# Performance work log

Measured on AMD Instinct MI355X. Metric: run time of the kernel, lower is better.

Reference implementation:

```python
import jax, jax.numpy as jnp
import numpy as np

T, C, H = 2048, 1024, 16
D = C // H  # head dim = 64


def setup_inputs() -> dict:
    key = jax.random.key(0)
    k1, k2, k3 = jax.random.split(key, 3)
    x = jax.random.normal(k1, (T, C), dtype=jnp.float32)
    W_qkv = jax.random.normal(k2, (C, 3 * C), dtype=jnp.float32) * (1.0 / np.sqrt(C))
    b_qkv = jnp.zeros((3 * C,), dtype=jnp.float32)
    W_proj = jax.random.normal(k3, (C, C), dtype=jnp.float32) * (1.0 / np.sqrt(C))
    b_proj = jnp.zeros((C,), dtype=jnp.float32)
    return {"x": x, "W_qkv": W_qkv, "b_qkv": b_qkv, "W_proj": W_proj, "b_proj": b_proj}


def reference(x, W_qkv, b_qkv, W_proj, b_proj):
    t, c = x.shape
    qkv = x @ W_qkv + b_qkv                      # [T, 3C] fused QKV projection
    q, k, v = jnp.split(qkv, 3, axis=-1)         # each [T, C]
    # split heads: [T, C] -> [H, T, D]
    q = q.reshape(t, H, D).transpose(1, 0, 2)
    k = k.reshape(t, H, D).transpose(1, 0, 2)
    v = v.reshape(t, H, D).transpose(1, 0, 2)
    # naive O(T^2) attention, full score matrix [H, T, T]
    att = jnp.einsum('htd,hsd->hts', q, k) / jnp.sqrt(jnp.float32(D))
    att = jax.nn.softmax(att, axis=-1)
    y = jnp.einsum('hts,hsd->htd', att, v)       # [H, T, D]
    y = y.transpose(1, 0, 2).reshape(t, c)       # merge heads -> [T, C]
    return y @ W_proj + b_proj
```

## Files before the change

### kernel.cpp

```cpp
#include <hip/hip_runtime.h>
#include <hip/hip_bf16.h>
#include <stdint.h>

#define T_DIM 2048
#define C_DIM 1024
#define H_DIM 16
#define D_HEAD 64
#define N_QKV 3072
#define CQ 0.18033688011112042f

typedef __bf16 bf16;
typedef __bf16 bf16x8 __attribute__((ext_vector_type(8)));
typedef __bf16 bf16x4 __attribute__((ext_vector_type(4)));
typedef __bf16 bf16x2 __attribute__((ext_vector_type(2)));
typedef float f32x4 __attribute__((ext_vector_type(4)));
typedef short s16x4 __attribute__((ext_vector_type(4)));

__device__ __forceinline__ void lds_load16(const void* g, void* l) {
    __builtin_amdgcn_global_load_lds(
        (const __attribute__((address_space(1))) void*)g,
        (__attribute__((address_space(3))) void*)l, 16, 0, 0);
}

__device__ __forceinline__ f32x4 mfma16(bf16x4 a, bf16x4 b, f32x4 c) {
#if __has_builtin(__builtin_amdgcn_mfma_f32_16x16x16_bf16)
    return __builtin_amdgcn_mfma_f32_16x16x16_bf16(a, b, c, 0, 0, 0);
#elif __has_builtin(__builtin_amdgcn_mfma_f32_16x16x16bf16_1k)
    union { bf16x4 v; s16x4 s; } ua, ub;
    ua.v = a; ub.v = b;
    return __builtin_amdgcn_mfma_f32_16x16x16bf16_1k(ua.s, ub.s, c, 0, 0, 0);
#else
    asm volatile("v_mfma_f32_16x16x16_bf16 %0, %1, %2, %0"
                 : "+v"(c) : "v"(a), "v"(b));
    return c;
#endif
}

__global__ void prep_kernel(const float* __restrict__ x, bf16* __restrict__ xb,
                            const float* __restrict__ Wq, bf16* __restrict__ WqT,
                            const float* __restrict__ Wp, bf16* __restrict__ WpT) {
    __shared__ float tile[32][33];
    int bid = blockIdx.x;
    int t = threadIdx.x;
    if (bid < 1024) {
        int i = (bid * 256 + t) * 8;
        float4 a = *(const float4*)(x + i);
        float4 b = *(const float4*)(x + i + 4);
        bf16x8 o;
        o[0] = (bf16)a.x; o[1] = (bf16)a.y; o[2] = (bf16)a.z; o[3] = (bf16)a.w;
        o[4] = (bf16)b.x; o[5] = (bf16)b.y; o[6] = (bf16)b.z; o[7] = (bf16)b.w;
        *(bf16x8*)(xb + i) = o;
        return;
    }
    bid -= 1024;
    const float* in; bf16* out; int N, nb, kb;
    if (bid < 3072) { in = Wq; out = WqT; N = N_QKV; nb = (bid % 96) * 32; kb = (bid / 96) * 32; }
    else { bid -= 3072; in = Wp; out = WpT; N = C_DIM; nb = (bid % 32) * 32; kb = (bid / 32) * 32; }
    int r = t >> 3, c4 = (t & 7) * 4;
    float4 v = *(const float4*)(in + (size_t)(kb + r) * N + nb + c4);
    tile[r][c4 + 0] = v.x; tile[r][c4 + 1] = v.y;
    tile[r][c4 + 2] = v.z; tile[r][c4 + 3] = v.w;
    __syncthreads();
    bf16x4 ov;
    ov[0] = (bf16)tile[c4 + 0][r]; ov[1] = (bf16)tile[c4 + 1][r];
    ov[2] = (bf16)tile[c4 + 2][r]; ov[3] = (bf16)tile[c4 + 3][r];
    *(bf16x4*)(out + (size_t)(nb + r) * C_DIM + kb + c4) = ov;
}

#define QKV_STAGE(BUF, K0) do {                                                      \
    lds_load16(ga + (K0),                            &As[BUF][0][(w * 16) * 32]);    \
    lds_load16(ga + (K0) + 32,                       &As[BUF][1][(w * 16) * 32]);    \
    lds_load16(ga + (size_t)64 * C_DIM + (K0),       &As[BUF][0][(64 + w * 16) * 32]); \
    lds_load16(ga + (size_t)64 * C_DIM + (K0) + 32,  &As[BUF][1][(64 + w * 16) * 32]); \
    lds_load16(gb + (K0),                            &Bs[BUF][0][(w * 16) * 32]);    \
    lds_load16(gb + (K0) + 32,                       &Bs[BUF][1][(w * 16) * 32]);    \
    lds_load16(gb + (size_t)64 * C_DIM + (K0),       &Bs[BUF][0][(64 + w * 16) * 32]); \
    lds_load16(gb + (size_t)64 * C_DIM + (K0) + 32,  &Bs[BUF][1][(64 + w * 16) * 32]); \
} while (0)

#define QKV_COMPUTE(BUF) do {                                                \
    _Pragma("unroll")                                                        \
    for (int p = 0; p < 2; ++p) {                                            \
        bf16x8 af[4], bfr[4];                                                \
        _Pragma("unroll")                                                    \
        for (int mi = 0; mi < 4; ++mi) af[mi]  = *(const bf16x8*)&As[BUF][p][(wm + mi * 16 + lo16) * 32 + quad * 8]; \
        _Pragma("unroll")                                                    \
        for (int ni = 0; ni < 4; ++ni) bfr[ni] = *(const bf16x8*)&Bs[BUF][p][(wn + ni * 16 + lo16) * 32 + quad * 8]; \
        _Pragma("unroll")                                                    \
        for (int mi = 0; mi < 4; ++mi)                                       \
            _Pragma("unroll")                                                \
            for (int ni = 0; ni < 4; ++ni)                                   \
                acc[mi][ni] = __builtin_amdgcn_mfma_f32_16x16x32_bf16(af[mi], bfr[ni], acc[mi][ni], 0, 0, 0); \
    }                                                                        \
} while (0)

#define WAIT_AND_BARRIER() do {                                              \
    asm volatile("s_waitcnt vmcnt(0)" ::: "memory");                         \
    __builtin_amdgcn_s_barrier();                                            \
} while (0)

__global__ __launch_bounds__(256, 2) void qkv_gemm_kernel(
    const bf16* __restrict__ A, const bf16* __restrict__ Bt,
    const float* __restrict__ bias, bf16* __restrict__ qkv)
{
    __shared__ __align__(16) bf16 As[2][2][128 * 32];
    __shared__ __align__(16) bf16 Bs[2][2][128 * 32];
    const int bid = blockIdx.x;
    const int xcd = bid & 7, slot = bid >> 3;
    const int rowBase = (slot / 3) * 128;
    const int colBase = (xcd * 3 + (slot % 3)) * 128;
    const int tid = threadIdx.x, lane = tid & 63, w = tid >> 6;
    const int lo16 = lane & 15, quad = lane >> 4;
    const int wm = (w & 1) * 64, wn = (w >> 1) * 64;

    const bf16* ga = A  + (size_t)(rowBase + w * 16 + (lane >> 2)) * C_DIM + (lane & 3) * 8;
    const bf16* gb = Bt + (size_t)(colBase + w * 16 + (lane >> 2)) * C_DIM + (lane & 3) * 8;

    f32x4 acc[4][4] = {};

    QKV_STAGE(0, 0);
    WAIT_AND_BARRIER();

    for (int k0 = 0; k0 < C_DIM; k0 += 128) {
        QKV_STAGE(1, k0 + 64);
        QKV_COMPUTE(0);
        WAIT_AND_BARRIER();
        if (k0 + 128 < C_DIM) QKV_STAGE(0, k0 + 128);
        QKV_COMPUTE(1);
        WAIT_AND_BARRIER();
    }

    const float scale = (colBase < C_DIM) ? CQ : 1.0f;
    #pragma unroll
    for (int ni = 0; ni < 4; ++ni) {
        int col = colBase + wn + ni * 16 + lo16;
        float bv = bias[col];
        #pragma unroll
        for (int mi = 0; mi < 4; ++mi) {
            int row0 = rowBase + wm + mi * 16 + quad * 4;
            #pragma unroll
            for (int r = 0; r < 4; ++r)
                qkv[(size_t)(row0 + r) * N_QKV + col] = (bf16)((acc[mi][ni][r] + bv) * scale);
        }
    }
}

__global__ __launch_bounds__(512, 2) void flash_kernel(
    const bf16* __restrict__ qkv,
    bf16* __restrict__ y)
{
    __shared__ union {
        __align__(16) bf16 Vt[4][64][38];
        float Ored[8][16][66];
    } u;
    __shared__ float lred[8][64];

    const int bid = blockIdx.x;
    const int xcd = bid & 7, slot = bid >> 3;
    const int h = xcd * 2 + (slot & 1);
    const int qb = slot >> 1;
    const int tid  = threadIdx.x;
    const int lane = tid & 63, w = tid >> 6;
    const int lo16 = lane & 15, quad = lane >> 4;

    bf16x8 qf[4][2];
    #pragma unroll
    for (int nq = 0; nq < 4; ++nq)
        #pragma unroll
        for (int dk = 0; dk < 2; ++dk)
            qf[nq][dk] = *(const bf16x8*)(qkv + (size_t)(qb * 64 + nq * 16 + lo16) * N_QKV
                                          + h * D_HEAD + dk * 32 + quad * 8);

    f32x4 o_t[4][4] = {};
    f32x4 o_l[4] = {};
    bf16x4 ones1;
    ones1[0] = (bf16)1.0f; ones1[1] = (bf16)1.0f; ones1[2] = (bf16)1.0f; ones1[3] = (bf16)1.0f;

    const bf16* kfb = qkv + (size_t)(w * 16 + lo16) * N_QKV + C_DIM + h * D_HEAD + quad * 8;
    const unsigned short* vb16 = (const unsigned short*)(qkv + 2 * C_DIM + h * D_HEAD);

    bf16x8 kf0 = *(const bf16x8*)(kfb);
    bf16x8 kf1 = *(const bf16x8*)(kfb + 32);
    unsigned short vreg[16];
    #pragma unroll
    for (int i = 0; i < 16; ++i)
        vreg[i] = vb16[(size_t)(w * 16 + i) * N_QKV + lane];

    bf16* vdst = &u.Vt[w >> 1][lane][(w & 1) * 16];

    for (int kt = 0; kt < T_DIM / 128; ++kt) {
        union { bf16x8 v; unsigned short us[8]; } p0, p1;
        #pragma unroll
        for (int i = 0; i < 8; ++i) { p0.us[i] = vreg[i]; p1.us[i] = vreg[8 + i]; }
        *(bf16x8*)vdst       = p0.v;
        *(bf16x8*)(vdst + 8) = p1.v;

        bf16x4 vf[4];
        #pragma unroll
        for (int mi = 0; mi < 4; ++mi)
            vf[mi] = *(const bf16x4*)&u.Vt[w >> 1][mi * 16 + lo16][(w & 1) * 16 + quad * 4];

        bf16x8 nkf0 = kf0, nkf1 = kf1;
        if (kt + 1 < T_DIM / 128) {
            const bf16* kp = kfb + (size_t)(kt + 1) * 128 * N_QKV;
            nkf0 = *(const bf16x8*)(kp);
            nkf1 = *(const bf16x8*)(kp + 32);
            #pragma unroll
            for (int i = 0; i < 16; ++i)
                vreg[i] = vb16[(size_t)((kt + 1) * 128 + w * 16 + i) * N_QKV + lane];
        }

        f32x4 st[4];
        #pragma unroll
        for (int nq = 0; nq < 4; ++nq) {
            f32x4 z = {};
            z = __builtin_amdgcn_mfma_f32_16x16x32_bf16(kf0, qf[nq][0], z, 0, 0, 0);
            st[nq] = __builtin_amdgcn_mfma_f32_16x16x32_bf16(kf1, qf[nq][1], z, 0, 0, 0);
        }

        bf16x4 pb[4];
        #pragma unroll
        for (int nq = 0; nq < 4; ++nq)
            #pragma unroll
            for (int r = 0; r < 4; ++r)
                pb[nq][r] = (bf16)__builtin_amdgcn_exp2f(st[nq][r]);

        __builtin_amdgcn_s_setprio(1);
        #pragma unroll
        for (int nq = 0; nq < 4; ++nq)
            o_l[nq] = mfma16(ones1, pb[nq], o_l[nq]);
        #pragma unroll
        for (int mi = 0; mi < 4; ++mi)
            #pragma unroll
            for (int nq = 0; nq < 4; ++nq)
                o_t[mi][nq] = mfma16(vf[mi], pb[nq], o_t[mi][nq]);
        __builtin_amdgcn_s_setprio(0);

        kf0 = nkf0; kf1 = nkf1;
    }

    #pragma unroll
    for (int nq = 0; nq < 4; ++nq)
        if (quad == 0) lred[w][nq * 16 + lo16] = o_l[nq][0];

    const int q8 = tid >> 3, dh = tid & 7;
    float linv = 0.f;
    #pragma unroll
    for (int mi = 0; mi < 4; ++mi) {
        __syncthreads();
        #pragma unroll
        for (int nq = 0; nq < 4; ++nq)
            #pragma unroll
            for (int r = 0; r < 4; ++r)
                u.Ored[w][quad * 4 + r][nq * 16 + lo16] = o_t[mi][nq][r];
        __syncthreads();
        if (mi == 0) {
            float ls = 0.f;
            #pragma unroll
            for (int j = 0; j < 8; ++j) ls += lred[j][q8];
            linv = 1.0f / ls;
        }
        bf16x2 ov;
        #pragma unroll
        for (int dj = 0; dj < 2; ++dj) {
            int d = dh * 2 + dj;
            float s = 0.f;
            #pragma unroll
            for (int j = 0; j < 8; ++j) s += u.Ored[j][d][q8];
            ov[dj] = (bf16)(s * linv);
        }
        *(bf16x2*)&y[(size_t)(qb * 64 + q8) * C_DIM + h * D_HEAD + mi * 16 + dh * 2] = ov;
    }
}

#define PROJ_STAGE(BUF, K0) do {                                             \
    lds_load16(ga + (K0),      &As[BUF][0][(w * 16) * 32]);                  \
    lds_load16(ga + (K0) + 32, &As[BUF][1][(w * 16) * 32]);                  \
    lds_load16(gb + (K0),      &Bs[BUF][0][(w * 16) * 32]);                  \
    lds_load16(gb + (K0) + 32, &Bs[BUF][1][(w * 16) * 32]);                  \
} while (0)

#define PROJ_COMPUTE(BUF) do {                                               \
    _Pragma("unroll")                                                        \
    for (int p = 0; p < 2; ++p) {                                            \
        bf16x8 af[2], bfr[2];                                                \
        _Pragma("unroll")                                                    \
        for (int mi = 0; mi < 2; ++mi) af[mi]  = *(const bf16x8*)&As[BUF][p][(wm + mi * 16 + lo16) * 32 + quad * 8]; \
        _Pragma("unroll")                                                    \
        for (int ni = 0; ni < 2; ++ni) bfr[ni] = *(const bf16x8*)&Bs[BUF][p][(wn + ni * 16 + lo16) * 32 + quad * 8]; \
        _Pragma("unroll")                                                    \
        for (int mi = 0; mi < 2; ++mi)                                       \
            _Pragma("unroll")                                                \
            for (int ni = 0; ni < 2; ++ni)                                   \
                acc[mi][ni] = __builtin_amdgcn_mfma_f32_16x16x32_bf16(af[mi], bfr[ni], acc[mi][ni], 0, 0, 0); \
    }                                                                        \
} while (0)

__global__ __launch_bounds__(256, 4) void proj_gemm_kernel(
    const bf16* __restrict__ A, const bf16* __restrict__ Bt,
    const float* __restrict__ bias, float* __restrict__ out)
{
    __shared__ __align__(16) bf16 As[2][2][64 * 32];
    __shared__ __align__(16) bf16 Bs[2][2][64 * 32];
    const int bid = blockIdx.x;
    const int xcd = bid & 7, slot = bid >> 3;
    const int colBase = (xcd * 2 + (slot & 1)) * 64;
    const int rowBase = (slot >> 1) * 64;
    const int tid = threadIdx.x, lane = tid & 63, w = tid >> 6;
    const int lo16 = lane & 15, quad = lane >> 4;
    const int wm = (w & 1) * 32, wn = (w >> 1) * 32;

    const bf16* ga = A  + (size_t)(rowBase + w * 16 + (lane >> 2)) * C_DIM + (lane & 3) * 8;
    const bf16* gb = Bt + (size_t)(colBase + w * 16 + (lane >> 2)) * C_DIM + (lane & 3) * 8;

    f32x4 acc[2][2] = {};

    PROJ_STAGE(0, 0);
    WAIT_AND_BARRIER();

    for (int k0 = 0; k0 < C_DIM; k0 += 128) {
        PROJ_STAGE(1, k0 + 64);
        PROJ_COMPUTE(0);
        WAIT_AND_BARRIER();
        if (k0 + 128 < C_DIM) PROJ_STAGE(0, k0 + 128);
        PROJ_COMPUTE(1);
        WAIT_AND_BARRIER();
    }

    #pragma unroll
    for (int ni = 0; ni < 2; ++ni) {
        int col = colBase + wn + ni * 16 + lo16;
        float bv = bias[col];
        #pragma unroll
        for (int mi = 0; mi < 2; ++mi) {
            int row0 = rowBase + wm + mi * 16 + quad * 4;
            #pragma unroll
            for (int r = 0; r < 4; ++r)
                out[(size_t)(row0 + r) * C_DIM + col] = acc[mi][ni][r] + bv;
        }
    }
}

extern "C" void kernel_launch(void* const* d_in, const int* in_sizes, int n_in,
                              void* d_out, int out_size, void* d_ws, size_t ws_size,
                              hipStream_t stream) {
    const float* x      = (const float*)d_in[0];
    const float* W_qkv  = (const float*)d_in[1];
    const float* b_qkv  = (const float*)d_in[2];
    const float* W_proj = (const float*)d_in[3];
    const float* b_proj = (const float*)d_in[4];
    float* out = (float*)d_out;

    char* ws = (char*)d_ws;
    bf16* xb      = (bf16*)(ws);
    bf16* Wqkv_t  = (bf16*)(ws + (4  << 20));
    bf16* Wproj_t = (bf16*)(ws + (10 << 20));
    bf16* qkv_bf  = (bf16*)(ws + (12 << 20));
    bf16* yb      = (bf16*)(ws + (24 << 20));

    prep_kernel<<<5120, 256, 0, stream>>>(x, xb, W_qkv, Wqkv_t, W_proj, Wproj_t);

    qkv_gemm_kernel<<<384, 256, 0, stream>>>(xb, Wqkv_t, b_qkv, qkv_bf);

    flash_kernel<<<512, 512, 0, stream>>>(qkv_bf, yb);

    proj_gemm_kernel<<<512, 256, 0, stream>>>(yb, Wproj_t, b_proj, out);
}
```

Measured before the change: 145.3 us.

## Move W_proj transpose into flash kernel tail blocks and widen prep transpose tiles

The W_proj fp32-to-bf16 transpose moves out of the prep kernel and into 256 extra blocks appended to the flash attention launch, so it runs alongside attention instead of on the critical path before the QKV GEMM. The remaining W_qkv transpose in prep now uses 64x64 tiles with 16-element vector writes, which cuts the block count and gives wider stores. The cost is a larger shared tile in prep and extra divergent blocks in flash that take part of the shared-memory union, which could affect flash occupancy.

```diff
diff --git a/kernel.cpp b/kernel.cpp
--- a/kernel.cpp
+++ b/kernel.cpp
@@ -37,9 +37,8 @@
 }
 
 __global__ void prep_kernel(const float* __restrict__ x, bf16* __restrict__ xb,
-                            const float* __restrict__ Wq, bf16* __restrict__ WqT,
-                            const float* __restrict__ Wp, bf16* __restrict__ WpT) {
-    __shared__ float tile[32][33];
+                            const float* __restrict__ Wq, bf16* __restrict__ WqT) {
+    __shared__ float tile[64][65];
     int bid = blockIdx.x;
     int t = threadIdx.x;
     if (bid < 1024) {
@@ -52,19 +51,28 @@
         *(bf16x8*)(xb + i) = o;
         return;
     }
-    bid -= 1024;
-    const float* in; bf16* out; int N, nb, kb;
-    if (bid < 3072) { in = Wq; out = WqT; N = N_QKV; nb = (bid % 96) * 32; kb = (bid / 96) * 32; }
-    else { bid -= 3072; in = Wp; out = WpT; N = C_DIM; nb = (bid % 32) * 32; kb = (bid / 32) * 32; }
-    int r = t >> 3, c4 = (t & 7) * 4;
-    float4 v = *(const float4*)(in + (size_t)(kb + r) * N + nb + c4);
-    tile[r][c4 + 0] = v.x; tile[r][c4 + 1] = v.y;
-    tile[r][c4 + 2] = v.z; tile[r][c4 + 3] = v.w;
+    int b2 = bid - 1024;
+    int nb = (b2 % 48) * 64, kb = (b2 / 48) * 64;
+    {
+        int r = t >> 2, c16 = (t & 3) * 16;
+        const float* src = Wq + (size_t)(kb + r) * N_QKV + nb + c16;
+        #pragma unroll
+        for (int j = 0; j < 4; ++j) {
+            float4 v = *(const float4*)(src + j * 4);
+            tile[r][c16 + j * 4 + 0] = v.x; tile[r][c16 + j * 4 + 1] = v.y;
+            tile[r][c16 + j * 4 + 2] = v.z; tile[r][c16 + j * 4 + 3] = v.w;
+        }
+    }
     __syncthreads();
-    bf16x4 ov;
-    ov[0] = (bf16)tile[c4 + 0][r]; ov[1] = (bf16)tile[c4 + 1][r];
-    ov[2] = (bf16)tile[c4 + 2][r]; ov[3] = (bf16)tile[c4 + 3][r];
-    *(bf16x4*)(out + (size_t)(nb + r) * C_DIM + kb + c4) = ov;
+    {
+        int n = t >> 2, s = (t & 3) * 16;
+        bf16x8 o0, o1;
+        #pragma unroll
+        for (int j = 0; j < 8; ++j) { o0[j] = (bf16)tile[s + j][n]; o1[j] = (bf16)tile[s + 8 + j][n]; }
+        bf16* dst = WqT + (size_t)(nb + n) * C_DIM + kb + s;
+        *(bf16x8*)(dst)     = o0;
+        *(bf16x8*)(dst + 8) = o1;
+    }
 }
 
 #define QKV_STAGE(BUF, K0) do {                                                      \
@@ -147,19 +155,47 @@
 
 __global__ __launch_bounds__(512, 2) void flash_kernel(
     const bf16* __restrict__ qkv,
+    const float* __restrict__ Wp,
+    bf16* __restrict__ WpT,
     bf16* __restrict__ y)
 {
     __shared__ union {
         __align__(16) bf16 Vt[4][64][38];
         float Ored[8][16][66];
+        float tile[64][66];
     } u;
     __shared__ float lred[8][64];
 
     const int bid = blockIdx.x;
+    const int tid  = threadIdx.x;
+
+    if (bid >= 512) {
+        int b2 = bid - 512;
+        int nb = (b2 & 15) * 64, kb = (b2 >> 4) * 64;
+        {
+            int r = tid >> 3, c8 = (tid & 7) * 8;
+            const float* src = Wp + (size_t)(kb + r) * C_DIM + nb + c8;
+            float4 a = *(const float4*)(src);
+            float4 b = *(const float4*)(src + 4);
+            u.tile[r][c8 + 0] = a.x; u.tile[r][c8 + 1] = a.y;
+            u.tile[r][c8 + 2] = a.z; u.tile[r][c8 + 3] = a.w;
+            u.tile[r][c8 + 4] = b.x; u.tile[r][c8 + 5] = b.y;
+            u.tile[r][c8 + 6] = b.z; u.tile[r][c8 + 7] = b.w;
+        }
+        __syncthreads();
+        {
+            int n = tid >> 3, s = (tid & 7) * 8;
+            bf16x8 ov;
+            #pragma unroll
+            for (int j = 0; j < 8; ++j) ov[j] = (bf16)u.tile[s + j][n];
+            *(bf16x8*)(WpT + (size_t)(nb + n) * C_DIM + kb + s) = ov;
+        }
+        return;
+    }
+
     const int xcd = bid & 7, slot = bid >> 3;
     const int h = xcd * 2 + (slot & 1);
     const int qb = slot >> 1;
-    const int tid  = threadIdx.x;
     const int lane = tid & 63, w = tid >> 6;
     const int lo16 = lane & 15, quad = lane >> 4;
 
@@ -358,11 +394,11 @@
     bf16* qkv_bf  = (bf16*)(ws + (12 << 20));
     bf16* yb      = (bf16*)(ws + (24 << 20));
 
-    prep_kernel<<<5120, 256, 0, stream>>>(x, xb, W_qkv, Wqkv_t, W_proj, Wproj_t);
+    prep_kernel<<<1792, 256, 0, stream>>>(x, xb, W_qkv, Wqkv_t);
 
     qkv_gemm_kernel<<<384, 256, 0, stream>>>(xb, Wqkv_t, b_qkv, qkv_bf);
 
-    flash_kernel<<<512, 512, 0, stream>>>(qkv_bf, yb);
+    flash_kernel<<<768, 512, 0, stream>>>(qkv_bf, W_proj, Wproj_t, yb);
 
     proj_gemm_kernel<<<512, 256, 0, stream>>>(yb, Wproj_t, b_proj, out);
 }
```

New measurement: 148.1 us. No clear change (+1.9%).
